# Kernel tuning notes

Measured on AMD Instinct MI355X. Metric: run time of the kernel, lower is better.

## Reference

```python
import jax, jax.numpy as jnp
import numpy as np

T = 100000   # timesteps (hourly)
WIN = 336    # window_size, hardcoded by Tanh(336,336)/Linear(336,out)
OUT = 48     # output_size (2-day horizon)
S = 168      # seasonality_2 (weekly)


def setup_inputs() -> dict:
    key = jax.random.key(0)
    ks = jax.random.split(key, 8)
    # strictly positive series (logs/divisions in forward)
    x = jax.random.uniform(ks[0], (T,), minval=0.5, maxval=1.5, dtype=jnp.float32)
    lvl_coef = jax.random.uniform(ks[1], (), minval=-1.0, maxval=1.0, dtype=jnp.float32)
    seas_coef = jax.random.uniform(ks[2], (), minval=-1.0, maxval=1.0, dtype=jnp.float32)
    # torch init: seasonality param p ~ U(0.65,1.35), used as exp(p); store raw p
    seas_params = jnp.log(jax.random.uniform(ks[3], (S,), minval=0.65, maxval=1.35, dtype=jnp.float32))
    W_tanh = jax.random.normal(ks[4], (WIN, WIN), dtype=jnp.float32) * 0.05
    b_tanh = jnp.zeros((WIN,), dtype=jnp.float32)
    W_out = jax.random.normal(ks[5], (WIN, OUT), dtype=jnp.float32) * 0.05
    b_out = jnp.zeros((OUT,), dtype=jnp.float32)
    return dict(x=x, lvl_coef=lvl_coef, seas_coef=seas_coef, seas_params=seas_params,
                W_tanh=W_tanh, b_tanh=b_tanh, W_out=W_out, b_out=b_out,
                window_size=WIN, output_size=OUT, lvp=50)


def reference(x, lvl_coef, seas_coef, seas_params, W_tanh, b_tanh, W_out, b_out,
              window_size, output_size, lvp):
    std = 0.001
    Tn = x.shape[0]
    a = jax.nn.sigmoid(lvl_coef)       # level smoothing
    g = jax.nn.sigmoid(seas_coef)      # seasonality smoothing
    w0 = jnp.exp(seas_params)          # initial weekly seasonality, [S]
    level0 = x[0] / w0[0]
    # w_seasons[1..S] = [w0[1], ..., w0[S-1], w0[0]] (torch appends w_seasons[0])
    buf0 = jnp.concatenate([w0[1:], w0[:1]])

    def step(carry, xi):
        level, buf = carry
        season = buf[0]                              # w_seasons[i], lag-S recurrence
        new_level = a * xi / season + (1.0 - a) * level
        new_season = g * xi / new_level + (1.0 - g) * season
        buf = jnp.concatenate([buf[1:], new_season[None]])
        return (new_level, buf), (new_level, new_season)

    _, (lvl_seq, new_seasons) = jax.lax.scan(step, (level0, buf0), x[1:])
    levels = jnp.concatenate([level0[None], lvl_seq])          # [T]
    w_all = jnp.concatenate([w0, w0[:1], new_seasons])[:Tn]    # w_seasons[0..T-1]

    # level variation penalty (torch builds it via torch.tensor(list) -> detached)
    lld = jnp.log(levels[1:] / levels[:-1])
    level_var_loss = jax.lax.stop_gradient(jnp.mean((lld[1:] - lld[:-1]) ** 2) * lvp)

    # vectorized sliding windows
    N = Tn - window_size - output_size + 1
    base = jnp.arange(N)
    iw = base[:, None] + jnp.arange(window_size)[None, :]
    il = base[:, None] + window_size + jnp.arange(output_size)[None, :]  # [N, OUT]
    lev = levels[base + window_size][:, None]                            # [N, 1]
    k1, k2 = jax.random.split(jax.random.key(1))
    inputs = jnp.log(x[iw] / (lev * w_all[iw])) + std * jax.random.normal(k1, (N, window_size), dtype=x.dtype)
    labels = jnp.log(x[il] / (lev * w_all[il])) + std * jax.random.normal(k2, (N, output_size), dtype=x.dtype)

    # skip_lstm head: Tanh(336,336) (linear + tanh) -> Linear(336, output_size)
    out = jnp.tanh(inputs @ W_tanh + b_tanh) @ W_out + b_out
    return out, labels, level_var_loss
```

## Files before the change

### kernel.cpp

```cpp
#include <hip/hip_runtime.h>
#include <hip/hip_bf16.h>

#define T_WIN 336
#define T_OUT 48
#define T_S   168
#define BM    128
#define CH    782

typedef __attribute__((ext_vector_type(8))) short short8;
typedef __attribute__((ext_vector_type(4))) float f32x4;

__device__ __forceinline__ short f2bf(float f) {
    union { float f; unsigned u; } v; v.f = f;
    unsigned r = v.u + 0x7FFFu + ((v.u >> 16) & 1u);
    return (short)(r >> 16);
}

template <int CTRL, int RMASK>
__device__ __forceinline__ float dppf(float v) {
    union { float f; int i; } in, out;
    in.f = v;
    out.i = __builtin_amdgcn_update_dpp(0, in.i, CTRL, RMASK, 0xf, true);
    return out.f;
}

__device__ __forceinline__ void st_wt(float* p, float v) {
    __hip_atomic_store(p, v, __ATOMIC_RELAXED, __HIP_MEMORY_SCOPE_AGENT);
}
__device__ __forceinline__ void st_wt_u(unsigned* p, unsigned v) {
    __hip_atomic_store(p, v, __ATOMIC_RELAXED, __HIP_MEMORY_SCOPE_AGENT);
}

__global__ void init_flags(int* flags) {
    if (threadIdx.x < 3) flags[threadIdx.x * 32] = 0;
}

__global__ __launch_bounds__(256, 2) void fused_kernel(
    const float* __restrict__ x, const float* __restrict__ lvl_coef,
    const float* __restrict__ seas_coef, const float* __restrict__ seas_params,
    const float* __restrict__ W1, const float* __restrict__ W2,
    const float* __restrict__ b1, const float* __restrict__ b2,
    short* __restrict__ W1F, short* __restrict__ W2F,
    float* __restrict__ w_all, float* __restrict__ levels,
    float* __restrict__ cs, float* __restrict__ outp,
    float* __restrict__ lab, float* __restrict__ lpart,
    int* flags, int T, int N, int NB)
{
    __shared__ float Lsf[512];
    __shared__ __align__(16) short Lbf0[512];
    __shared__ __align__(16) short Lbf1[512];
    __shared__ float llv[BM];
    __shared__ __align__(16) short hs[BM * 72];
    __shared__ __align__(16) short B1s[11 * 4 * 512];
    __shared__ __align__(16) short B2s[6 * 512];
    __shared__ int sh_tk;

    int blk = blockIdx.x;
    int tid = threadIdx.x;
    int* progress  = flags;
    int* prep_done = flags + 32;
    int* ticket    = flags + 64;

    if (blk == 0) {
        if (tid >= 64) return;
        __builtin_amdgcn_s_setprio(3);
        int lane = tid;
        float a = 1.f / (1.f + __expf(-lvl_coef[0]));
        float g = 1.f / (1.f + __expf(-seas_coef[0]));
        float q = 1.f - a, gq = 1.f - g;

        for (int t = lane; t < T_S + 1; t += 64) w_all[t] = __expf(seas_params[t % T_S]);
        float lvl = x[0] / __expf(seas_params[0]);
        if (lane == 0) levels[0] = lvl;

        float wcur[3];
        #pragma unroll
        for (int i = 0; i < 3; ++i)
            wcur[i] = __expf(seas_params[(1 + 3 * lane + i) % T_S]);

        float f1 = q * q * q;
        float f2 = f1 * f1, f4 = f2 * f2, f8 = f4 * f4;
        float lnq = __logf(q);
        float P15 = __expf(3.f * (float)((lane & 15) + 1) * lnq);
        float P31 = __expf(3.f * (float)((lane & 31) + 1) * lnq);
        float pw3l = __expf(3.f * (float)lane * lnq);

        int j0 = 3 * lane;

        auto do_chunk = [&](const float* xvv, float* lev) {
            float rr[3];
            #pragma unroll
            for (int i = 0; i < 3; ++i) rr[i] = a * xvv[i] * __builtin_amdgcn_rcpf(wcur[i]);
            float S = fmaf(q, fmaf(q, rr[0], rr[1]), rr[2]);
            S = fmaf(f1, dppf<0x111, 0xf>(S), S);
            S = fmaf(f2, dppf<0x112, 0xf>(S), S);
            S = fmaf(f4, dppf<0x114, 0xf>(S), S);
            S = fmaf(f8, dppf<0x118, 0xf>(S), S);
            S = fmaf(P15, dppf<0x142, 0xa>(S), S);
            S = fmaf(P31, dppf<0x143, 0xc>(S), S);
            float E = dppf<0x138, 0xf>(S);
            float lv = fmaf(pw3l, lvl, E);
            #pragma unroll
            for (int i = 0; i < 3; ++i) { lv = fmaf(q, lv, rr[i]); lev[i] = lv; }
            { union { float f; int i; } uu; uu.i = __builtin_amdgcn_readlane(__builtin_bit_cast(int, lev[2]), 55); lvl = uu.f; }
            #pragma unroll
            for (int i = 0; i < 3; ++i)
                wcur[i] = fmaf(gq, wcur[i], g * xvv[i] * __builtin_amdgcn_rcpf(lev[i]));
        };

        float xg[4][3], xh[4][3], x2[4][3];
        #pragma unroll
        for (int u = 0; u < 4; ++u)
            #pragma unroll
            for (int i = 0; i < 3; ++i) {
                xg[u][i] = x[1 + T_S * u + j0 + i];
                xh[u][i] = x[1 + T_S * (4 + u) + j0 + i];
            }

        const float* px = x + 1 + 8 * T_S + j0;
        float* pl = levels + 1 + j0;
        float* pw = w_all + 1 + T_S + j0;

        for (int grp = 0; grp < 148; ++grp) {
            if (grp && (grp & 7) == 0 && lane == 0)
                __hip_atomic_store(progress, grp, __ATOMIC_RELEASE, __HIP_MEMORY_SCOPE_AGENT);

            if (grp < 146) {
                #pragma unroll
                for (int u = 0; u < 4; ++u)
                    #pragma unroll
                    for (int i = 0; i < 3; ++i)
                        x2[u][i] = px[u * T_S + i];
            } else {
                #pragma unroll
                for (int u = 0; u < 4; ++u)
                    #pragma unroll
                    for (int i = 0; i < 3; ++i) {
                        int t = 1 + T_S * (4 * (grp + 2) + u) + j0 + i;
                        x2[u][i] = x[min(t, T - 1)];
                    }
            }
            px += 4 * T_S;

            #pragma unroll
            for (int u = 0; u < 4; ++u) {
                float lev[3];
                do_chunk(xg[u], lev);
                #pragma unroll
                for (int i = 0; i < 3; ++i) {
                    pl[u * T_S + i] = lev[i];
                    pw[u * T_S + i] = wcur[i];
                }
            }
            pl += 4 * T_S; pw += 4 * T_S;
            #pragma unroll
            for (int u = 0; u < 4; ++u)
                #pragma unroll
                for (int i = 0; i < 3; ++i) { xg[u][i] = xh[u][i]; xh[u][i] = x2[u][i]; }
        }

        #pragma unroll
        for (int u = 0; u < 4; ++u) {
            int c = 592 + u;
            if (c * T_S >= T - 1) break;
            int len = (T - 1) - T_S * c; if (len > T_S) len = T_S;
            float lev[3];
            do_chunk(xg[u], lev);
            #pragma unroll
            for (int i = 0; i < 3; ++i) {
                if (j0 + i < len) {
                    pl[u * T_S + i] = lev[i];
                    pw[u * T_S + i] = wcur[i];
                }
            }
        }
        if (lane == 0)
            __hip_atomic_store(progress, 1000, __ATOMIC_RELEASE, __HIP_MEMORY_SCOPE_AGENT);
        return;
    }

    if (blk <= 302) {
        if (blk >= 301) {
            int k = (blk - 301) * 256 + tid;
            if (k < T_WIN) {
                float s = 0.f;
                for (int j = 0; j < T_WIN; ++j) s += W1[j * T_WIN + k];
                st_wt(&cs[k], s);
            }
        } else if (blk >= 265) {
            int d = (blk - 265) * 256 + tid;
            int j2 = d & 3, lane = (d >> 2) & 63, f = d >> 8;
            int ct2 = f % 3, rest = f / 3;
            int kt2 = rest & 1, c = rest >> 1;
            int k = c * 64 + kt2 * 32 + (lane >> 4) * 8 + 2 * j2;
            int o = ct2 * 16 + (lane & 15);
            unsigned short lo = 0, hi = 0;
            if (k     < T_WIN) lo = (unsigned short)f2bf(W2[k * T_OUT + o]);
            if (k + 1 < T_WIN) hi = (unsigned short)f2bf(W2[(k + 1) * T_OUT + o]);
            st_wt_u(&((unsigned*)W2F)[d], ((unsigned)hi << 16) | (unsigned)lo);
        } else {
            int d = (blk - 1) * 256 + tid;
            int j2 = d & 3, lane = (d >> 2) & 63, f = d >> 8;
            int ct = f & 3, rest = f >> 2;
            int kt = rest % 11, c = rest / 11;
            int k = kt * 32 + (lane >> 4) * 8 + 2 * j2;
            int col = c * 64 + ct * 16 + (lane & 15);
            unsigned short lo = 0, hi = 0;
            if (col < T_WIN) {
                if (k     < T_WIN) lo = (unsigned short)f2bf(W1[k * T_WIN + col]);
                if (k + 1 < T_WIN) hi = (unsigned short)f2bf(W1[(k + 1) * T_WIN + col]);
            }
            st_wt_u(&((unsigned*)W1F)[d], ((unsigned)hi << 16) | (unsigned)lo);
        }
        __syncthreads();
        if (tid == 0)
            __hip_atomic_fetch_add(prep_done, 1, __ATOMIC_RELAXED, __HIP_MEMORY_SCOPE_AGENT);
    }

    if (tid < 64) {
        while (__hip_atomic_load(prep_done, __ATOMIC_RELAXED, __HIP_MEMORY_SCOPE_AGENT) < 302)
            __builtin_amdgcn_s_sleep(16);
    }
    __syncthreads();

    int lane = tid & 63, wv = tid >> 6;
    int lr = lane & 15, lq = lane >> 4;
    int rw = wv * 32;
    int last_seen = 0;
    int NT = NB + 128;

    for (;;) {
        __syncthreads();
        if (tid == 0) sh_tk = atomicAdd(ticket, 1);
        __syncthreads();
        int tk = sh_tk;
        if (tk >= NT) return;

        int sev = tk / 7;
        bool isl = (tk % 7 == 6) && (sev < 128);
        int tile = isl ? (NB + sev) : (tk - min(sev, 128));

        int need_t = (tile < NB) ? (tile * BM + 512 + 128)
                                 : ((tile - NB) * CH + CH + 2 + 128);
        if (need_t > T) need_t = T;
        int req = (need_t + 670) / 672;
        if (last_seen < req) {
            if (tid < 64) {
                while (__hip_atomic_load(progress, __ATOMIC_RELAXED, __HIP_MEMORY_SCOPE_AGENT) < req)
                    __builtin_amdgcn_s_sleep(32);
            }
            __syncthreads();
            last_seen = req;
        }

        if (tile >= NB) {
            float* ls  = (float*)hs;
            float* red = (float*)(hs + 4096);
            int lb = tile - NB;
            int lo = lb * CH;
            int n = T - lo; if (n > CH + 2) n = CH + 2;
            for (int i = tid; i < n; i += 256) ls[i] = __logf(levels[lo + i]);
            __syncthreads();
            float s = 0.f;
            int dmax = (T - 2) - lo; if (dmax > CH) dmax = CH;
            for (int i = tid; i < dmax; i += 256) {
                float d = ls[i + 2] - 2.f * ls[i + 1] + ls[i];
                s = fmaf(d, d, s);
            }
            red[tid] = s;
            __syncthreads();
            for (int w = 128; w > 0; w >>= 1) {
                if (tid < w) red[tid] += red[tid + w];
                __syncthreads();
            }
            if (tid == 0) lpart[lb] = red[0];
            continue;
        }

        int n0 = tile * BM;
        float C = __logf(levels[min(n0 + T_WIN, T - 1)]);

        for (int i = tid; i < 512; i += 256) {
            int t = n0 + i;
            float v = (t < T) ? (__logf(x[t]) - __logf(w_all[t]) - C) : 0.f;
            Lsf[i] = v;
            Lbf0[i] = f2bf(v);
        }
        for (int i = tid; i < BM; i += 256) {
            int t = n0 + i + T_WIN;
            llv[i] = (t < T) ? (__logf(levels[t]) - C) : 0.f;
        }
        __syncthreads();
        for (int i = tid; i < 512; i += 256) Lbf1[i] = (i < 511) ? Lbf0[i + 1] : (short)0;
        __syncthreads();

        for (int u2 = tid; u2 < BM * T_OUT; u2 += 256) {
            int row = u2 / T_OUT, j = u2 - row * T_OUT;
            int nn = n0 + row;
            if (nn < N) lab[(size_t)nn * T_OUT + j] = Lsf[row + T_WIN + j] - llv[row];
        }

        const short* abase = ((lr & 1) ? Lbf1 : Lbf0) + rw + (lr & ~1);
        short8 af[11][2];
        #pragma unroll
        for (int kt = 0; kt < 11; ++kt) {
            #pragma unroll
            for (int mt = 0; mt < 2; ++mt) {
                const int* ip = (const int*)(abase + mt * 16 + kt * 32 + lq * 8);
                union { short8 s; int i[4]; } u;
                u.i[0] = ip[0]; u.i[1] = ip[1]; u.i[2] = ip[2]; u.i[3] = ip[3];
                af[kt][mt] = u.s;
            }
        }

        f32x4 zero4 = {0.f, 0.f, 0.f, 0.f};
        f32x4 acc2[2][3];
        #pragma unroll
        for (int mt = 0; mt < 2; ++mt)
            #pragma unroll
            for (int ct = 0; ct < 3; ++ct) acc2[mt][ct] = zero4;

        #pragma unroll 1
        for (int c = 0; c < 6; ++c) {
            __syncthreads();

            const char* g1 = (const char*)(W1F + (size_t)c * 11 * 4 * 512);
            for (int seg = wv; seg < 44; seg += 4) {
                __builtin_amdgcn_global_load_lds(
                    (const __attribute__((address_space(1))) unsigned int*)(g1 + seg * 1024 + lane * 16),
                    (__attribute__((address_space(3))) unsigned int*)((char*)B1s + seg * 1024),
                    16, 0, 0);
            }
            const char* g2 = (const char*)(W2F + (size_t)c * 6 * 512);
            for (int seg = wv; seg < 6; seg += 4) {
                __builtin_amdgcn_global_load_lds(
                    (const __attribute__((address_space(1))) unsigned int*)(g2 + seg * 1024 + lane * 16),
                    (__attribute__((address_space(3))) unsigned int*)((char*)B2s + seg * 1024),
                    16, 0, 0);
            }
            float b1v[4], csv[4];
            #pragma unroll
            for (int ct = 0; ct < 4; ++ct) {
                int col = c * 64 + ct * 16 + lr;
                b1v[ct] = (col < T_WIN) ? b1[col] : 0.f;
                csv[ct] = (col < T_WIN) ? cs[col] : 0.f;
            }
            __syncthreads();

            f32x4 acc1[2][4];
            #pragma unroll
            for (int mt = 0; mt < 2; ++mt)
                #pragma unroll
                for (int ct = 0; ct < 4; ++ct) acc1[mt][ct] = zero4;

            #pragma unroll
            for (int kt = 0; kt < 11; ++kt) {
                #pragma unroll
                for (int ct = 0; ct < 4; ++ct) {
                    short8 bf = *(const short8*)&B1s[((kt * 4 + ct) * 64 + lane) * 8];
                    acc1[0][ct] = __builtin_amdgcn_mfma_f32_16x16x32_bf16(af[kt][0], bf, acc1[0][ct], 0, 0, 0);
                    acc1[1][ct] = __builtin_amdgcn_mfma_f32_16x16x32_bf16(af[kt][1], bf, acc1[1][ct], 0, 0, 0);
                }
            }

            #pragma unroll
            for (int mt = 0; mt < 2; ++mt)
                #pragma unroll
                for (int ct = 0; ct < 4; ++ct)
                    #pragma unroll
                    for (int r = 0; r < 4; ++r) {
                        int row = rw + mt * 16 + lq * 4 + r;
                        float pre = acc1[mt][ct][r] + b1v[ct] - llv[row] * csv[ct];
                        float e = __expf(2.f * pre);
                        float h = 1.f - 2.f * __builtin_amdgcn_rcpf(e + 1.f);
                        hs[row * 72 + ct * 16 + lr] = f2bf(h);
                    }

            #pragma unroll
            for (int kt2 = 0; kt2 < 2; ++kt2) {
                short8 a2[2];
                #pragma unroll
                for (int mt = 0; mt < 2; ++mt)
                    a2[mt] = *(const short8*)&hs[(rw + mt * 16 + lr) * 72 + kt2 * 32 + lq * 8];
                #pragma unroll
                for (int ct2 = 0; ct2 < 3; ++ct2) {
                    short8 bf2 = *(const short8*)&B2s[((kt2 * 3 + ct2) * 64 + lane) * 8];
                    acc2[0][ct2] = __builtin_amdgcn_mfma_f32_16x16x32_bf16(a2[0], bf2, acc2[0][ct2], 0, 0, 0);
                    acc2[1][ct2] = __builtin_amdgcn_mfma_f32_16x16x32_bf16(a2[1], bf2, acc2[1][ct2], 0, 0, 0);
                }
            }
        }

        float b2v[3];
        #pragma unroll
        for (int ct2 = 0; ct2 < 3; ++ct2) b2v[ct2] = b2[ct2 * 16 + lr];
        #pragma unroll
        for (int mt = 0; mt < 2; ++mt)
            #pragma unroll
            for (int ct2 = 0; ct2 < 3; ++ct2)
                #pragma unroll
                for (int r = 0; r < 4; ++r) {
                    int row = n0 + rw + mt * 16 + lq * 4 + r;
                    if (row < N)
                        outp[(size_t)row * T_OUT + ct2 * 16 + lr] = acc2[mt][ct2][r] + b2v[ct2];
                }
    }
}

__global__ __launch_bounds__(128) void loss2_kernel(
    const float* __restrict__ part, const int* __restrict__ lvp,
    float* __restrict__ out_loss, int T)
{
    __shared__ float red[128];
    red[threadIdx.x] = part[threadIdx.x];
    __syncthreads();
    for (int w = 64; w > 0; w >>= 1) {
        if (threadIdx.x < (unsigned)w) red[threadIdx.x] += red[threadIdx.x + w];
        __syncthreads();
    }
    if (threadIdx.x == 0) out_loss[0] = red[0] * (float)lvp[0] / (float)(T - 2);
}

extern "C" void kernel_launch(void* const* d_in, const int* in_sizes, int n_in,
                              void* d_out, int out_size, void* d_ws, size_t ws_size,
                              hipStream_t stream) {
    const float* x    = (const float*)d_in[0];
    const float* lvlc = (const float*)d_in[1];
    const float* seac = (const float*)d_in[2];
    const float* sp   = (const float*)d_in[3];
    const float* W1   = (const float*)d_in[4];
    const float* b1   = (const float*)d_in[5];
    const float* W2   = (const float*)d_in[6];
    const float* b2   = (const float*)d_in[7];
    const int*   lvp  = (const int*)d_in[10];

    int T = in_sizes[0];
    int N = T - T_WIN - T_OUT + 1;
    int NB = (N + BM - 1) / BM;

    short* W1F    = (short*)d_ws;
    short* W2F    = W1F + 264 * 512;
    float* w_all  = (float*)(W2F + 36 * 512);
    float* levels = w_all + T + 192;
    float* cs     = levels + T;
    float* lpart  = cs + 352;
    int*   flagsp = (int*)(lpart + 128);

    float* outp  = (float*)d_out;
    float* lab   = outp + (size_t)N * T_OUT;
    float* lossp = lab + (size_t)N * T_OUT;

    init_flags<<<1, 64, 0, stream>>>(flagsp);
    fused_kernel<<<512, 256, 0, stream>>>(x, lvlc, seac, sp, W1, W2, b1, b2,
                                          W1F, W2F, w_all, levels, cs,
                                          outp, lab, lpart, flagsp, T, N, NB);
    loss2_kernel<<<1, 128, 0, stream>>>(lpart, lvp, lossp, T);
}
```

Measured before the change: 230.3 us.

## Load MFMA B fragments directly from global with register prefetch, drop LDS staging

Weight fragments for both GEMMs are now read straight from global memory (L2-resident, pre-swizzled) into registers, with the next k-slice prefetched one step ahead. This removes the per-chunk LDS staging buffers and their two block barriers. It also frees about 50KB of LDS, which could raise occupancy. Label stores move after the GEMM and, like the output and loss-partial stores, go through a write-through/streaming store helper. The cost is more global/L2 traffic per wave, since each wave now fetches its own copy of the weights, plus higher register pressure from the prefetch buffers.

```diff
diff --git a/kernel.cpp b/kernel.cpp
--- a/kernel.cpp
+++ b/kernel.cpp
@@ -51,8 +51,6 @@
     __shared__ __align__(16) short Lbf1[512];
     __shared__ float llv[BM];
     __shared__ __align__(16) short hs[BM * 72];
-    __shared__ __align__(16) short B1s[11 * 4 * 512];
-    __shared__ __align__(16) short B2s[6 * 512];
     __shared__ int sh_tk;
 
     int blk = blockIdx.x;
@@ -273,7 +271,7 @@
                 if (tid < w) red[tid] += red[tid + w];
                 __syncthreads();
             }
-            if (tid == 0) lpart[lb] = red[0];
+            if (tid == 0) st_wt(&lpart[lb], red[0]);
             continue;
         }
 
@@ -294,12 +292,6 @@
         for (int i = tid; i < 512; i += 256) Lbf1[i] = (i < 511) ? Lbf0[i + 1] : (short)0;
         __syncthreads();
 
-        for (int u2 = tid; u2 < BM * T_OUT; u2 += 256) {
-            int row = u2 / T_OUT, j = u2 - row * T_OUT;
-            int nn = n0 + row;
-            if (nn < N) lab[(size_t)nn * T_OUT + j] = Lsf[row + T_WIN + j] - llv[row];
-        }
-
         const short* abase = ((lr & 1) ? Lbf1 : Lbf0) + rw + (lr & ~1);
         short8 af[11][2];
         #pragma unroll
@@ -322,22 +314,9 @@
 
         #pragma unroll 1
         for (int c = 0; c < 6; ++c) {
-            __syncthreads();
-
-            const char* g1 = (const char*)(W1F + (size_t)c * 11 * 4 * 512);
-            for (int seg = wv; seg < 44; seg += 4) {
-                __builtin_amdgcn_global_load_lds(
-                    (const __attribute__((address_space(1))) unsigned int*)(g1 + seg * 1024 + lane * 16),
-                    (__attribute__((address_space(3))) unsigned int*)((char*)B1s + seg * 1024),
-                    16, 0, 0);
-            }
-            const char* g2 = (const char*)(W2F + (size_t)c * 6 * 512);
-            for (int seg = wv; seg < 6; seg += 4) {
-                __builtin_amdgcn_global_load_lds(
-                    (const __attribute__((address_space(1))) unsigned int*)(g2 + seg * 1024 + lane * 16),
-                    (__attribute__((address_space(3))) unsigned int*)((char*)B2s + seg * 1024),
-                    16, 0, 0);
-            }
+            const char* g1 = (const char*)(W1F + (size_t)c * 11 * 4 * 512) + lane * 16;
+            const char* g2 = (const char*)(W2F + (size_t)c * 6 * 512) + lane * 16;
+
             float b1v[4], csv[4];
             #pragma unroll
             for (int ct = 0; ct < 4; ++ct) {
@@ -345,7 +324,6 @@
                 b1v[ct] = (col < T_WIN) ? b1[col] : 0.f;
                 csv[ct] = (col < T_WIN) ? cs[col] : 0.f;
             }
-            __syncthreads();
 
             f32x4 acc1[2][4];
             #pragma unroll
@@ -353,14 +331,24 @@
                 #pragma unroll
                 for (int ct = 0; ct < 4; ++ct) acc1[mt][ct] = zero4;
 
+            short8 bcur[4], bnxt[4];
+            #pragma unroll
+            for (int ct = 0; ct < 4; ++ct)
+                bcur[ct] = *(const short8*)(g1 + ct * 1024);
             #pragma unroll
             for (int kt = 0; kt < 11; ++kt) {
+                if (kt < 10) {
+                    #pragma unroll
+                    for (int ct = 0; ct < 4; ++ct)
+                        bnxt[ct] = *(const short8*)(g1 + ((kt + 1) * 4 + ct) * 1024);
+                }
                 #pragma unroll
                 for (int ct = 0; ct < 4; ++ct) {
-                    short8 bf = *(const short8*)&B1s[((kt * 4 + ct) * 64 + lane) * 8];
-                    acc1[0][ct] = __builtin_amdgcn_mfma_f32_16x16x32_bf16(af[kt][0], bf, acc1[0][ct], 0, 0, 0);
-                    acc1[1][ct] = __builtin_amdgcn_mfma_f32_16x16x32_bf16(af[kt][1], bf, acc1[1][ct], 0, 0, 0);
-                }
+                    acc1[0][ct] = __builtin_amdgcn_mfma_f32_16x16x32_bf16(af[kt][0], bcur[ct], acc1[0][ct], 0, 0, 0);
+                    acc1[1][ct] = __builtin_amdgcn_mfma_f32_16x16x32_bf16(af[kt][1], bcur[ct], acc1[1][ct], 0, 0, 0);
+                }
+                #pragma unroll
+                for (int ct = 0; ct < 4; ++ct) bcur[ct] = bnxt[ct];
             }
 
             #pragma unroll
@@ -384,11 +372,17 @@
                     a2[mt] = *(const short8*)&hs[(rw + mt * 16 + lr) * 72 + kt2 * 32 + lq * 8];
                 #pragma unroll
                 for (int ct2 = 0; ct2 < 3; ++ct2) {
-                    short8 bf2 = *(const short8*)&B2s[((kt2 * 3 + ct2) * 64 + lane) * 8];
+                    short8 bf2 = *(const short8*)(g2 + (kt2 * 3 + ct2) * 1024);
                     acc2[0][ct2] = __builtin_amdgcn_mfma_f32_16x16x32_bf16(a2[0], bf2, acc2[0][ct2], 0, 0, 0);
                     acc2[1][ct2] = __builtin_amdgcn_mfma_f32_16x16x32_bf16(a2[1], bf2, acc2[1][ct2], 0, 0, 0);
                 }
             }
+        }
+
+        for (int u2 = tid; u2 < BM * T_OUT; u2 += 256) {
+            int row = u2 / T_OUT, j = u2 - row * T_OUT;
+            int nn = n0 + row;
+            if (nn < N) st_wt(&lab[(size_t)nn * T_OUT + j], Lsf[row + T_WIN + j] - llv[row]);
         }
 
         float b2v[3];
@@ -402,7 +396,7 @@
                 for (int r = 0; r < 4; ++r) {
                     int row = n0 + rw + mt * 16 + lq * 4 + r;
                     if (row < N)
-                        outp[(size_t)row * T_OUT + ct2 * 16 + lr] = acc2[mt][ct2][r] + b2v[ct2];
+                        st_wt(&outp[(size_t)row * T_OUT + ct2 * 16 + lr], acc2[mt][ct2][r] + b2v[ct2]);
                 }
     }
 }
```

Result: slower. 244.4 us (+6.1%).
